# Performance work log

Measured on AMD Instinct MI355X. Metric: run time of the kernel, lower is better.

Reference implementation:

```python
import jax, jax.numpy as jnp
import numpy as np

B, T, I, H = 32, 512, 512, 512  # batch, seq_len, input_size, hidden_size


def setup_inputs() -> dict:
    key = jax.random.key(0)
    ks = jax.random.split(key, 9)
    s = 1.0 / np.sqrt(H)  # PyTorch LSTM init: U(-1/sqrt(H), 1/sqrt(H))
    u = lambda k, shape: jax.random.uniform(k, shape, jnp.float32, -s, s)
    return {
        "x": jax.random.normal(ks[0], (B, T, I), jnp.float32),
        "h0": jnp.zeros((2, B, H), jnp.float32),
        "c0": jnp.zeros((2, B, H), jnp.float32),
        "w_ih_f": u(ks[1], (4 * H, I)), "w_hh_f": u(ks[2], (4 * H, H)),
        "b_ih_f": u(ks[3], (4 * H,)), "b_hh_f": u(ks[4], (4 * H,)),
        "w_ih_r": u(ks[5], (4 * H, I)), "w_hh_r": u(ks[6], (4 * H, H)),
        "b_ih_r": u(ks[7], (4 * H,)), "b_hh_r": u(ks[8], (4 * H,)),
    }


def _lstm_dir(x, h0, c0, w_ih, w_hh, b_ih, b_hh):
    # Precompute input projections for all timesteps: [T, B, 4H] (time-major for scan).
    gx = jnp.einsum('bti,gi->tbg', x, w_ih) + b_ih + b_hh

    def step(carry, g):
        h, c = carry
        g = g + h @ w_hh.T  # [B, 4H]
        i, f, gg, o = jnp.split(g, 4, axis=-1)  # PyTorch gate order: i, f, g, o
        c = jax.nn.sigmoid(f) * c + jax.nn.sigmoid(i) * jnp.tanh(gg)
        h = jax.nn.sigmoid(o) * jnp.tanh(c)
        return (h, c), h

    (hT, cT), hs = jax.lax.scan(step, (h0, c0), gx)
    return hs.transpose(1, 0, 2), hT, cT  # [B, T, H], [B, H], [B, H]


def reference(x, h0, c0, w_ih_f, w_hh_f, b_ih_f, b_hh_f,
              w_ih_r, w_hh_r, b_ih_r, b_hh_r):
    out_f, hT_f, cT_f = _lstm_dir(x, h0[0], c0[0], w_ih_f, w_hh_f, b_ih_f, b_hh_f)
    out_r, hT_r, cT_r = _lstm_dir(x[:, ::-1], h0[1], c0[1], w_ih_r, w_hh_r, b_ih_r, b_hh_r)
    out = jnp.concatenate([out_f, out_r[:, ::-1]], axis=-1)  # [B, T, 2H]
    h_n = jnp.stack([hT_f, hT_r])  # [2, B, H]
    c_n = jnp.stack([cT_f, cT_r])  # [2, B, H]
    return out, h_n, c_n
```

## Files before the change

### kernel.cpp

```cpp
#include <hip/hip_runtime.h>
#include <hip/hip_bf16.h>
#include <math.h>
#include <stdint.h>

#define BB 32
#define TT 512
#define II 512
#define HH 512
#define G4 (4 * HH)
#define MM (TT * BB)
#define BH (BB * HH)
#define WGD 32

typedef __hip_bfloat16 bf16;
typedef __attribute__((ext_vector_type(8))) short short8;
typedef __attribute__((ext_vector_type(4))) float f32x4;
typedef __attribute__((ext_vector_type(4))) unsigned u32x4;

__device__ __forceinline__ float bf2f(bf16 v) { return __bfloat162float(v); }
__device__ __forceinline__ bf16  f2bf(float v) { return __float2bfloat16(v); }
__device__ __forceinline__ short f2bs(float x) { bf16 v = f2bf(x); return *reinterpret_cast<short*>(&v); }
__device__ __forceinline__ float bs2f(short s) {
    unsigned u = ((unsigned)(unsigned short)s) << 16;
    return __uint_as_float(u);
}
__device__ __forceinline__ short8 pk8(float4 u, float4 v) {
    short8 t;
    t[0] = f2bs(u.x); t[1] = f2bs(u.y); t[2] = f2bs(u.z); t[3] = f2bs(u.w);
    t[4] = f2bs(v.x); t[5] = f2bs(v.y); t[6] = f2bs(v.z); t[7] = f2bs(v.w);
    return t;
}

#define GX1 ((size_t)TT * 4 * 128 * 128)

__global__ __launch_bounds__(256) void proj_mfma_kernel(
    const float* __restrict__ x,
    const float* __restrict__ w_f, const float* __restrict__ w_r,
    const float* __restrict__ bi_f, const float* __restrict__ bh_f,
    const float* __restrict__ bi_r, const float* __restrict__ bh_r,
    bf16* __restrict__ gx, int dir0)
{
    const int dl = blockIdx.z, dir = dir0 + dl;
    const int m0 = blockIdx.x * 64;
    const int n0 = blockIdx.y * 128;
    const float* __restrict__ w  = dir ? w_r  : w_f;
    const float* __restrict__ bi = dir ? bi_r : bi_f;
    const float* __restrict__ bh = dir ? bh_r : bh_f;

    __shared__ __align__(16) char smem[17408];
    bf16 (*As)[40]  = (bf16(*)[40])smem;
    bf16 (*Bs)[40]  = (bf16(*)[40])(smem + 5120);
    bf16 (*Cs)[136] = (bf16(*)[136])smem;

    const int tid = threadIdx.x;
    const int wv = tid >> 6, l = tid & 63;
    const int nl = l & 15, ko = (l >> 4) * 8;

    const int a_r = tid >> 2, a_s = tid & 3;
    const float* a_src = x + ((size_t)((m0 + a_r) & 31) * TT + (size_t)((m0 + a_r) >> 5)) * II + a_s * 8;
    const int b_r = tid >> 1, b_h = tid & 1;
    const float* b_src = w + (size_t)(n0 + b_r) * II + b_h * 16;

    f32x4 acc[8];
#pragma unroll
    for (int j = 0; j < 8; ++j) acc[j] = (f32x4){0.f, 0.f, 0.f, 0.f};

    float bias[8];
#pragma unroll
    for (int j = 0; j < 8; ++j) {
        const int n = n0 + j * 16 + nl;
        bias[j] = bi[n] + bh[n];
    }

    for (int k0 = 0; k0 < II; k0 += 32) {
        const float4 av0 = *(const float4*)(a_src + k0);
        const float4 av1 = *(const float4*)(a_src + k0 + 4);
        const float4 bv0 = *(const float4*)(b_src + k0);
        const float4 bv1 = *(const float4*)(b_src + k0 + 4);
        const float4 bv2 = *(const float4*)(b_src + k0 + 8);
        const float4 bv3 = *(const float4*)(b_src + k0 + 12);
        __syncthreads();
        *(short8*)&As[a_r][a_s * 8] = pk8(av0, av1);
        *(short8*)&Bs[b_r][b_h * 16]     = pk8(bv0, bv1);
        *(short8*)&Bs[b_r][b_h * 16 + 8] = pk8(bv2, bv3);
        __syncthreads();
        const short8 a = *(const short8*)&As[wv * 16 + nl][ko];
#pragma unroll
        for (int j = 0; j < 8; ++j) {
            const short8 b = *(const short8*)&Bs[j * 16 + nl][ko];
            acc[j] = __builtin_amdgcn_mfma_f32_16x16x32_bf16(a, b, acc[j], 0, 0, 0);
        }
    }

    __syncthreads();
    const int row0 = (l >> 4) * 4;
#pragma unroll
    for (int j = 0; j < 8; ++j)
#pragma unroll
        for (int r = 0; r < 4; ++r)
            Cs[wv * 16 + row0 + r][j * 16 + nl] = f2bf(acc[j][r] + bias[j]);
    __syncthreads();

    bf16* gxd = gx + (size_t)dl * GX1;
    const int g   = n0 >> 9;
    const int cgb = (n0 & 511) >> 2;
    const int t_base = blockIdx.x * 2;
#pragma unroll
    for (int i = 0; i < 4; ++i) {
        const int c = i * 256 + tid;
        const int tl = c >> 9, cgl = (c >> 4) & 31, u = c & 15;
        const int r0 = tl * 32 + 2 * u;
        const uint2 lo = *(const uint2*)&Cs[r0][cgl * 4];
        const uint2 hi = *(const uint2*)&Cs[r0 + 1][cgl * 4];
        uint4 ov; ov.x = lo.x; ov.y = lo.y; ov.z = hi.x; ov.w = hi.y;
        *(uint4*)(gxd + ((((size_t)(t_base + tl) * 4 + g) * 128 + cgb + cgl) * 128 + u * 8)) = ov;
    }
}

__global__ __launch_bounds__(256, 1) void lstm_rec_kernel(
    const bf16* __restrict__ gx,
    const float* __restrict__ h0, const float* __restrict__ c0,
    const float* __restrict__ whh_f, const float* __restrict__ whh_r,
    float* __restrict__ dout,
    bf16* __restrict__ h_buf,
    unsigned int* __restrict__ bars,
    int dir0)
{
    const int dl  = blockIdx.x >> 5;
    const int wgl = blockIdx.x & 31;
    const int dir = dir0 + dl;
    const int tid = threadIdx.x;
    const int wv  = tid >> 6;
    const int l   = tid & 63;
    const int cg  = wgl * 4 + wv;
    const int j0  = cg * 4;
    const float* __restrict__ whh = dir ? whh_r : whh_f;
    unsigned int* barsd = bars + (size_t)dl * 256;

    __shared__ __align__(16) bf16 h_s[32][520];
    __shared__ __align__(16) float ex[4][16][36];

    const int nl = l & 15;
    const int g  = nl >> 2, jj = nl & 3;
    const int ko = (l >> 4) * 8;

    short8 bfrag[16];
    {
        const float* wr = whh + ((size_t)g * HH + (size_t)(j0 + jj)) * HH;
#pragma unroll
        for (int ks = 0; ks < 16; ++ks) {
            const float* p = wr + ks * 32 + ko;
            short8 t;
#pragma unroll
            for (int i = 0; i < 8; ++i) t[i] = f2bs(p[i]);
            bfrag[ks] = t;
        }
    }

    const int mC = l >> 1;
    const int jjA = (l & 1) * 2;

    float cs0, cs1;
    {
        const float* cp = c0 + (size_t)dir * BH + (size_t)mC * HH + j0 + jjA;
        cs0 = cp[0]; cs1 = cp[1];
    }

    bf16* hsl = h_buf + (size_t)dl * 2 * BH;
    const unsigned* gxw = (const unsigned*)(gx + (size_t)dl * GX1);

    for (int q = 0; q < 64; ++q) {
        const int f = q * 256 + tid;
        h_s[f >> 9][f & 511] = f2bf(h0[(size_t)dir * BH + f]);
    }
    __syncthreads();

    unsigned gw[4];
    {
        const int t0 = dir ? (TT - 1) : 0;
#pragma unroll
        for (int gg = 0; gg < 4; ++gg)
            gw[gg] = gxw[((size_t)(t0 * 4 + gg) * 128 + cg) * 64 + l];
    }

#pragma unroll 1
    for (int s = 0; s < TT; ++s) {
        const int t_x = dir ? (TT - 1 - s) : s;

        f32x4 acc0 = {0.f, 0.f, 0.f, 0.f};
        f32x4 acc1 = {0.f, 0.f, 0.f, 0.f};
#pragma unroll
        for (int half = 0; half < 2; ++half) {
            short8 a0[8], a1[8];
#pragma unroll
            for (int k = 0; k < 8; ++k) {
                const int ks = half * 8 + k;
                a0[k] = *(const short8*)&h_s[nl][ks * 32 + ko];
                a1[k] = *(const short8*)&h_s[nl + 16][ks * 32 + ko];
            }
#pragma unroll
            for (int k = 0; k < 8; ++k) {
                acc0 = __builtin_amdgcn_mfma_f32_16x16x32_bf16(a0[k], bfrag[half * 8 + k], acc0, 0, 0, 0);
                acc1 = __builtin_amdgcn_mfma_f32_16x16x32_bf16(a1[k], bfrag[half * 8 + k], acc1, 0, 0, 0);
            }
        }

        {
            const int row0 = (l >> 4) * 4;
            *(f32x4*)&ex[wv][nl][row0]      = acc0;
            *(f32x4*)&ex[wv][nl][16 + row0] = acc1;
        }

        float hv0, hv1;
#pragma unroll
        for (int c = 0; c < 2; ++c) {
            const int jc = jjA + c;
            const int sh = 16 * c;
            float q0 = ex[wv][0 * 4 + jc][mC] + bs2f((short)(gw[0] >> sh));
            float q1 = ex[wv][1 * 4 + jc][mC] + bs2f((short)(gw[1] >> sh));
            float q2 = ex[wv][2 * 4 + jc][mC] + bs2f((short)(gw[2] >> sh));
            float q3 = ex[wv][3 * 4 + jc][mC] + bs2f((short)(gw[3] >> sh));
            q0 = fminf(fmaxf(q0, -30.f), 30.f);
            q1 = fminf(fmaxf(q1, -30.f), 30.f);
            q2 = fminf(fmaxf(q2, -30.f), 30.f);
            q3 = fminf(fmaxf(q3, -30.f), 30.f);
            const float ig = 1.f / (1.f + __expf(-q0));
            const float fg = 1.f / (1.f + __expf(-q1));
            const float te = __expf(2.f * q2);
            const float gg = (te - 1.f) / (te + 1.f);
            const float og = 1.f / (1.f + __expf(-q3));
            float cs = (c == 0) ? cs0 : cs1;
            cs = fg * cs + ig * gg;
            const float csc = fminf(fmaxf(cs, -15.f), 15.f);
            const float t2 = __expf(2.f * csc);
            const float th = (t2 - 1.f) / (t2 + 1.f);
            const float h = og * th;
            if (c == 0) { cs0 = cs; hv0 = h; } else { cs1 = cs; hv1 = h; }
        }

        if (s < TT - 1) {
            {
                bf16 hb0 = f2bf(hv0), hb1 = f2bf(hv1);
                unsigned pk = (unsigned)*(unsigned short*)&hb0 |
                              ((unsigned)*(unsigned short*)&hb1 << 16);
                unsigned* hp = (unsigned*)(hsl + (size_t)((s + 1) & 1) * BH + (size_t)mC * HH + j0 + jjA);
                __hip_atomic_store(hp, pk, __ATOMIC_RELAXED, __HIP_MEMORY_SCOPE_AGENT);
            }
            asm volatile("s_waitcnt vmcnt(0)" ::: "memory");
            __syncthreads();
            if (tid == 0)
                __hip_atomic_fetch_add(barsd + (wgl & 3) * 64, 1u,
                                       __ATOMIC_RELAXED, __HIP_MEMORY_SCOPE_AGENT);

            {
                float2 ho; ho.x = hv0; ho.y = hv1;
                *(float2*)(dout + ((size_t)mC * TT + t_x) * (2 * HH) + (size_t)dir * HH + j0 + jjA) = ho;
            }
            const int t_n = dir ? (TT - 2 - s) : (s + 1);
            unsigned gwn[4];
#pragma unroll
            for (int gg = 0; gg < 4; ++gg)
                gwn[gg] = gxw[((size_t)(t_n * 4 + gg) * 128 + cg) * 64 + l];

            if (wv == 0 && l < 4) {
                const unsigned tgt = (unsigned)(WGD / 4) * (unsigned)(s + 1);
                while (__hip_atomic_load(barsd + l * 64,
                                         __ATOMIC_RELAXED, __HIP_MEMORY_SCOPE_AGENT) < tgt) {
                    __builtin_amdgcn_s_sleep(1);
                }
            }
            __syncthreads();

            {
                const u32x4* src = (const u32x4*)(hsl + (size_t)((s + 1) & 1) * BH);
                u32x4 vv[8];
#pragma unroll
                for (int q = 0; q < 8; ++q) {
                    const u32x4* p = src + (q * 256 + tid);
                    asm volatile("global_load_dwordx4 %0, %1, off sc0 sc1"
                                 : "=v"(vv[q]) : "v"(p));
                }
                asm volatile("s_waitcnt vmcnt(0)" ::: "memory");
#pragma unroll
                for (int q = 0; q < 8; ++q) {
                    const int e = (q * 256 + tid) * 8;
                    *(u32x4*)&h_s[e >> 9][e & 511] = vv[q];
                }
            }
            __syncthreads();
#pragma unroll
            for (int gg = 0; gg < 4; ++gg) gw[gg] = gwn[gg];
        } else {
            float2 ho; ho.x = hv0; ho.y = hv1;
            *(float2*)(dout + ((size_t)mC * TT + t_x) * (2 * HH) + (size_t)dir * HH + j0 + jjA) = ho;
            const size_t hn_off = (size_t)BB * TT * 2 * HH;
            float2 co; co.x = cs0; co.y = cs1;
            *(float2*)(dout + hn_off + (size_t)dir * BH + (size_t)mC * HH + j0 + jjA) = ho;
            *(float2*)(dout + hn_off + 2 * (size_t)BH + (size_t)dir * BH + (size_t)mC * HH + j0 + jjA) = co;
        }
    }
}

extern "C" void kernel_launch(void* const* d_in, const int* in_sizes, int n_in,
                              void* d_out, int out_size, void* d_ws, size_t ws_size,
                              hipStream_t stream)
{
    (void)in_sizes; (void)n_in; (void)out_size;
    const float* x     = (const float*)d_in[0];
    const float* h0    = (const float*)d_in[1];
    const float* c0    = (const float*)d_in[2];
    const float* wih_f = (const float*)d_in[3];
    const float* whh_f = (const float*)d_in[4];
    const float* bih_f = (const float*)d_in[5];
    const float* bhh_f = (const float*)d_in[6];
    const float* wih_r = (const float*)d_in[7];
    const float* whh_r = (const float*)d_in[8];
    const float* bih_r = (const float*)d_in[9];
    const float* bhh_r = (const float*)d_in[10];
    float* out = (float*)d_out;

    const size_t gx1 = GX1 * sizeof(bf16);
    const size_t needA = 2 * gx1 + (size_t)4 * BH * sizeof(bf16) + 4096;
    char* ws = (char*)d_ws;

    if (ws_size >= needA) {
        bf16* gx = (bf16*)ws;
        bf16* h_buf = (bf16*)(ws + 2 * gx1);
        unsigned int* bars = (unsigned int*)(ws + 2 * gx1 + (size_t)4 * BH * sizeof(bf16));
        hipMemsetAsync(bars, 0, 2048, stream);
        dim3 g1(MM / 64, G4 / 128, 2);
        proj_mfma_kernel<<<g1, 256, 0, stream>>>(x, wih_f, wih_r, bih_f, bhh_f, bih_r, bhh_r, gx, 0);
        lstm_rec_kernel<<<dim3(2 * WGD), dim3(256), 0, stream>>>(
            gx, h0, c0, whh_f, whh_r, out, h_buf, bars, 0);
    } else {
        bf16* gx = (bf16*)ws;
        bf16* h_buf = (bf16*)(ws + gx1);
        unsigned int* bars = (unsigned int*)(ws + gx1 + (size_t)2 * BH * sizeof(bf16));
        for (int d = 0; d < 2; ++d) {
            hipMemsetAsync(bars, 0, 2048, stream);
            dim3 g1(MM / 64, G4 / 128, 1);
            proj_mfma_kernel<<<g1, 256, 0, stream>>>(x, wih_f, wih_r, bih_f, bhh_f, bih_r, bhh_r, gx, d);
            lstm_rec_kernel<<<dim3(WGD), dim3(256), 0, stream>>>(
                gx, h0, c0, whh_f, whh_r, out, h_buf, bars, d);
        }
    }
}
```

Before: 1.867 ms.

## Replace per-step grid barrier with step-tagged ring buffer and flag polling

Each hidden-state pair is stored together with its step number in an 8-slot ring in global memory. Consumers poll those tags directly instead of waiting on a per-step atomic counter barrier, and the full barrier now runs only once every 8 steps to stop slots from being overwritten too early. The goal is to take the grid-wide barrier round trip off the critical path of each recurrence step. In exchange, each exchanged element doubles in size and polling can re-issue loads, which adds memory traffic.

```diff
diff --git a/kernel.cpp b/kernel.cpp
--- a/kernel.cpp
+++ b/kernel.cpp
@@ -11,6 +11,10 @@
 #define MM (TT * BB)
 #define BH (BB * HH)
 #define WGD 32
+
+#define SLOTS 8
+#define PAIRS 8192
+#define RING1 ((size_t)SLOTS * PAIRS * 8)
 
 typedef __hip_bfloat16 bf16;
 typedef __attribute__((ext_vector_type(8))) short short8;
@@ -122,7 +126,7 @@
     const float* __restrict__ h0, const float* __restrict__ c0,
     const float* __restrict__ whh_f, const float* __restrict__ whh_r,
     float* __restrict__ dout,
-    bf16* __restrict__ h_buf,
+    unsigned long long* __restrict__ ring,
     unsigned int* __restrict__ bars,
     int dir0)
 {
@@ -135,6 +139,7 @@
     const int cg  = wgl * 4 + wv;
     const int j0  = cg * 4;
     const float* __restrict__ whh = dir ? whh_r : whh_f;
+    unsigned long long* ringd = ring + (size_t)dl * SLOTS * PAIRS;
     unsigned int* barsd = bars + (size_t)dl * 256;
 
     __shared__ __align__(16) bf16 h_s[32][520];
@@ -157,8 +162,10 @@
         }
     }
 
-    const int mC = l >> 1;
+    const int mC  = l >> 1;
     const int jjA = (l & 1) * 2;
+    const int pc_own = cg * 2 + (l & 1);
+    const bool own_col = (((tid & 127) >> 2) == wgl);
 
     float cs0, cs1;
     {
@@ -166,7 +173,6 @@
         cs0 = cp[0]; cs1 = cp[1];
     }
 
-    bf16* hsl = h_buf + (size_t)dl * 2 * BH;
     const unsigned* gxw = (const unsigned*)(gx + (size_t)dl * GX1);
 
     for (int q = 0; q < 64; ++q) {
@@ -238,19 +244,20 @@
             if (c == 0) { cs0 = cs; hv0 = h; } else { cs1 = cs; hv1 = h; }
         }
 
+        __syncthreads();
+
         if (s < TT - 1) {
+            unsigned pk;
             {
                 bf16 hb0 = f2bf(hv0), hb1 = f2bf(hv1);
-                unsigned pk = (unsigned)*(unsigned short*)&hb0 |
-                              ((unsigned)*(unsigned short*)&hb1 << 16);
-                unsigned* hp = (unsigned*)(hsl + (size_t)((s + 1) & 1) * BH + (size_t)mC * HH + j0 + jjA);
-                __hip_atomic_store(hp, pk, __ATOMIC_RELAXED, __HIP_MEMORY_SCOPE_AGENT);
-            }
-            asm volatile("s_waitcnt vmcnt(0)" ::: "memory");
-            __syncthreads();
-            if (tid == 0)
-                __hip_atomic_fetch_add(barsd + (wgl & 3) * 64, 1u,
-                                       __ATOMIC_RELAXED, __HIP_MEMORY_SCOPE_AGENT);
+                pk = (unsigned)*(unsigned short*)&hb0 |
+                     ((unsigned)*(unsigned short*)&hb1 << 16);
+                const unsigned long long pk64 =
+                    (unsigned long long)pk | ((unsigned long long)(unsigned)(s + 1) << 32);
+                unsigned long long* hp =
+                    ringd + (size_t)((s + 1) & (SLOTS - 1)) * PAIRS + (size_t)mC * 256 + pc_own;
+                __hip_atomic_store(hp, pk64, __ATOMIC_RELAXED, __HIP_MEMORY_SCOPE_AGENT);
+            }
 
             {
                 float2 ho; ho.x = hv0; ho.y = hv1;
@@ -262,32 +269,53 @@
             for (int gg = 0; gg < 4; ++gg)
                 gwn[gg] = gxw[((size_t)(t_n * 4 + gg) * 128 + cg) * 64 + l];
 
-            if (wv == 0 && l < 4) {
-                const unsigned tgt = (unsigned)(WGD / 4) * (unsigned)(s + 1);
-                while (__hip_atomic_load(barsd + l * 64,
-                                         __ATOMIC_RELAXED, __HIP_MEMORY_SCOPE_AGENT) < tgt) {
-                    __builtin_amdgcn_s_sleep(1);
+            {
+                const unsigned expt = (unsigned)(s + 1);
+                const char* sb = (const char*)(ringd + (size_t)((s + 1) & (SLOTS - 1)) * PAIRS)
+                                 + (size_t)tid * 16;
+                const int row_h = tid >> 7;
+                const int bcol  = 4 * (tid & 127);
+                u32x4 vv[16];
+                unsigned need = own_col ? 0u : 0xffffu;
+                while (need) {
+#pragma unroll
+                    for (int q = 0; q < 16; ++q) {
+                        if (need & (1u << q)) {
+                            const char* p = sb + q * 4096;
+                            asm volatile("global_load_dwordx4 %0, %1, off sc0 sc1"
+                                         : "=v"(vv[q]) : "v"(p));
+                        }
+                    }
+                    asm volatile("s_waitcnt vmcnt(0)" ::: "memory");
+#pragma unroll
+                    for (int q = 0; q < 16; ++q) {
+                        if (need & (1u << q)) {
+                            if (vv[q][1] == expt && vv[q][3] == expt) {
+                                uint2 o; o.x = vv[q][0]; o.y = vv[q][2];
+                                *(uint2*)&h_s[2 * q + row_h][bcol] = o;
+                                need &= ~(1u << q);
+                            }
+                        }
+                    }
                 }
+                *(unsigned*)&h_s[mC][j0 + jjA] = pk;
             }
             __syncthreads();
 
-            {
-                const u32x4* src = (const u32x4*)(hsl + (size_t)((s + 1) & 1) * BH);
-                u32x4 vv[8];
-#pragma unroll
-                for (int q = 0; q < 8; ++q) {
-                    const u32x4* p = src + (q * 256 + tid);
-                    asm volatile("global_load_dwordx4 %0, %1, off sc0 sc1"
-                                 : "=v"(vv[q]) : "v"(p));
+            if (((s + 1) & (SLOTS - 1)) == 0) {
+                if (tid == 0)
+                    __hip_atomic_fetch_add(barsd + (wgl & 3) * 64, 1u,
+                                           __ATOMIC_RELAXED, __HIP_MEMORY_SCOPE_AGENT);
+                if (wv == 0 && l < 4) {
+                    const unsigned tgt = (unsigned)(WGD / 4) * (unsigned)((s + 1) >> 3);
+                    while (__hip_atomic_load(barsd + l * 64,
+                                             __ATOMIC_RELAXED, __HIP_MEMORY_SCOPE_AGENT) < tgt) {
+                        __builtin_amdgcn_s_sleep(1);
+                    }
                 }
-                asm volatile("s_waitcnt vmcnt(0)" ::: "memory");
-#pragma unroll
-                for (int q = 0; q < 8; ++q) {
-                    const int e = (q * 256 + tid) * 8;
-                    *(u32x4*)&h_s[e >> 9][e & 511] = vv[q];
-                }
-            }
-            __syncthreads();
+                __syncthreads();
+            }
+
 #pragma unroll
             for (int gg = 0; gg < 4; ++gg) gw[gg] = gwn[gg];
         } else {
@@ -320,28 +348,28 @@
     float* out = (float*)d_out;
 
     const size_t gx1 = GX1 * sizeof(bf16);
-    const size_t needA = 2 * gx1 + (size_t)4 * BH * sizeof(bf16) + 4096;
+    const size_t needA = 2 * gx1 + 2 * RING1 + 8192;
     char* ws = (char*)d_ws;
 
     if (ws_size >= needA) {
         bf16* gx = (bf16*)ws;
-        bf16* h_buf = (bf16*)(ws + 2 * gx1);
-        unsigned int* bars = (unsigned int*)(ws + 2 * gx1 + (size_t)4 * BH * sizeof(bf16));
-        hipMemsetAsync(bars, 0, 2048, stream);
+        unsigned long long* ring = (unsigned long long*)(ws + 2 * gx1);
+        unsigned int* bars = (unsigned int*)(ws + 2 * gx1 + 2 * RING1);
+        hipMemsetAsync(ring, 0, 2 * RING1 + 4096, stream);
         dim3 g1(MM / 64, G4 / 128, 2);
         proj_mfma_kernel<<<g1, 256, 0, stream>>>(x, wih_f, wih_r, bih_f, bhh_f, bih_r, bhh_r, gx, 0);
         lstm_rec_kernel<<<dim3(2 * WGD), dim3(256), 0, stream>>>(
-            gx, h0, c0, whh_f, whh_r, out, h_buf, bars, 0);
+            gx, h0, c0, whh_f, whh_r, out, ring, bars, 0);
     } else {
         bf16* gx = (bf16*)ws;
-        bf16* h_buf = (bf16*)(ws + gx1);
-        unsigned int* bars = (unsigned int*)(ws + gx1 + (size_t)2 * BH * sizeof(bf16));
+        unsigned long long* ring = (unsigned long long*)(ws + gx1);
+        unsigned int* bars = (unsigned int*)(ws + gx1 + RING1);
         for (int d = 0; d < 2; ++d) {
-            hipMemsetAsync(bars, 0, 2048, stream);
+            hipMemsetAsync(ring, 0, RING1 + 4096, stream);
             dim3 g1(MM / 64, G4 / 128, 1);
             proj_mfma_kernel<<<g1, 256, 0, stream>>>(x, wih_f, wih_r, bih_f, bhh_f, bih_r, bhh_r, gx, d);
             lstm_rec_kernel<<<dim3(WGD), dim3(256), 0, stream>>>(
-                gx, h0, c0, whh_f, whh_r, out, h_buf, bars, d);
-        }
-    }
-}
+                gx, h0, c0, whh_f, whh_r, out, ring, bars, d);
+        }
+    }
+}
```

Result: slower. 2.264 ms (+21.3%).

## Replace per-step grid barrier with NaN-sentinel ring buffer polling for hidden state

Applied to the files above, without the earlier changes.

Swaps the per-timestep atomic-counter grid barrier for a ring buffer with one slot per timestep. Each slot is pre-filled with bf16 NaN sentinels, and consumers poll the slot until every 16-byte chunk is non-NaN, so the counter round-trip and the spin-wait are gone from the critical path. Each workgroup writes its own chunk straight into LDS instead of reading it back. In exchange the kernel must initialise a much larger ring buffer up front, uses more workspace, and would misbehave if a real hidden value were the NaN pattern.

```diff
diff --git a/kernel.cpp b/kernel.cpp
--- a/kernel.cpp
+++ b/kernel.cpp
@@ -11,6 +11,11 @@
 #define MM (TT * BB)
 #define BH (BB * HH)
 #define WGD 32
+
+#define SLOT_DW (BH / 2)
+#define RING_DW ((size_t)TT * SLOT_DW)
+#define RING_BYTES (RING_DW * 4)
+#define NANP 0x7FC0u
 
 typedef __hip_bfloat16 bf16;
 typedef __attribute__((ext_vector_type(8))) short short8;
@@ -122,7 +127,7 @@
     const float* __restrict__ h0, const float* __restrict__ c0,
     const float* __restrict__ whh_f, const float* __restrict__ whh_r,
     float* __restrict__ dout,
-    bf16* __restrict__ h_buf,
+    unsigned* __restrict__ ring,
     unsigned int* __restrict__ bars,
     int dir0)
 {
@@ -135,6 +140,7 @@
     const int cg  = wgl * 4 + wv;
     const int j0  = cg * 4;
     const float* __restrict__ whh = dir ? whh_r : whh_f;
+    unsigned* ringd = ring + (size_t)dl * RING_DW;
     unsigned int* barsd = bars + (size_t)dl * 256;
 
     __shared__ __align__(16) bf16 h_s[32][520];
@@ -157,8 +163,9 @@
         }
     }
 
-    const int mC = l >> 1;
+    const int mC  = l >> 1;
     const int jjA = (l & 1) * 2;
+    const int poff = mC * 256 + ((j0 + jjA) >> 1);
 
     float cs0, cs1;
     {
@@ -166,13 +173,33 @@
         cs0 = cp[0]; cs1 = cp[1];
     }
 
-    bf16* hsl = h_buf + (size_t)dl * 2 * BH;
     const unsigned* gxw = (const unsigned*)(gx + (size_t)dl * GX1);
 
     for (int q = 0; q < 64; ++q) {
         const int f = q * 256 + tid;
         h_s[f >> 9][f & 511] = f2bf(h0[(size_t)dir * BH + f]);
     }
+
+    {
+        unsigned long long* rq = (unsigned long long*)ringd;
+        const int gt = wgl * 256 + tid;
+        const unsigned long long NN = 0x7FC07FC07FC07FC0ull;
+#pragma unroll 4
+        for (int q = 0; q < 256; ++q)
+            __hip_atomic_store(rq + (size_t)q * 8192 + gt, NN,
+                               __ATOMIC_RELAXED, __HIP_MEMORY_SCOPE_AGENT);
+        asm volatile("s_waitcnt vmcnt(0)" ::: "memory");
+    }
+    __syncthreads();
+    if (tid == 0)
+        __hip_atomic_fetch_add(barsd + (wgl & 3) * 64, 1u,
+                               __ATOMIC_RELAXED, __HIP_MEMORY_SCOPE_AGENT);
+    if (wv == 0 && l < 4) {
+        while (__hip_atomic_load(barsd + l * 64,
+                                 __ATOMIC_RELAXED, __HIP_MEMORY_SCOPE_AGENT) < (unsigned)(WGD / 4)) {
+            __builtin_amdgcn_s_sleep(1);
+        }
+    }
     __syncthreads();
 
     unsigned gw[4];
@@ -182,6 +209,8 @@
         for (int gg = 0; gg < 4; ++gg)
             gw[gg] = gxw[((size_t)(t0 * 4 + gg) * 128 + cg) * 64 + l];
     }
+
+    const unsigned need_init = (((tid & 63) >> 1) == wgl) ? 0u : 0xFFu;
 
 #pragma unroll 1
     for (int s = 0; s < TT; ++s) {
@@ -238,19 +267,19 @@
             if (c == 0) { cs0 = cs; hv0 = h; } else { cs1 = cs; hv1 = h; }
         }
 
+        __syncthreads();
+
         if (s < TT - 1) {
+            unsigned* slot = ringd + (size_t)(s + 1) * SLOT_DW;
+
+            unsigned pk;
             {
                 bf16 hb0 = f2bf(hv0), hb1 = f2bf(hv1);
-                unsigned pk = (unsigned)*(unsigned short*)&hb0 |
-                              ((unsigned)*(unsigned short*)&hb1 << 16);
-                unsigned* hp = (unsigned*)(hsl + (size_t)((s + 1) & 1) * BH + (size_t)mC * HH + j0 + jjA);
-                __hip_atomic_store(hp, pk, __ATOMIC_RELAXED, __HIP_MEMORY_SCOPE_AGENT);
-            }
-            asm volatile("s_waitcnt vmcnt(0)" ::: "memory");
-            __syncthreads();
-            if (tid == 0)
-                __hip_atomic_fetch_add(barsd + (wgl & 3) * 64, 1u,
-                                       __ATOMIC_RELAXED, __HIP_MEMORY_SCOPE_AGENT);
+                pk = (unsigned)*(unsigned short*)&hb0 |
+                     ((unsigned)*(unsigned short*)&hb1 << 16);
+                __hip_atomic_store(slot + poff, pk,
+                                   __ATOMIC_RELAXED, __HIP_MEMORY_SCOPE_AGENT);
+            }
 
             {
                 float2 ho; ho.x = hv0; ho.y = hv1;
@@ -262,30 +291,36 @@
             for (int gg = 0; gg < 4; ++gg)
                 gwn[gg] = gxw[((size_t)(t_n * 4 + gg) * 128 + cg) * 64 + l];
 
-            if (wv == 0 && l < 4) {
-                const unsigned tgt = (unsigned)(WGD / 4) * (unsigned)(s + 1);
-                while (__hip_atomic_load(barsd + l * 64,
-                                         __ATOMIC_RELAXED, __HIP_MEMORY_SCOPE_AGENT) < tgt) {
-                    __builtin_amdgcn_s_sleep(1);
+            {
+                u32x4 vv[8];
+                unsigned need = need_init;
+                while (need) {
+#pragma unroll
+                    for (int q = 0; q < 8; ++q) {
+                        if (need & (1u << q)) {
+                            const unsigned* p = slot + (q * 256 + tid) * 4;
+                            asm volatile("global_load_dwordx4 %0, %1, off sc0 sc1"
+                                         : "=v"(vv[q]) : "v"(p));
+                        }
+                    }
+                    asm volatile("s_waitcnt vmcnt(0)" ::: "memory");
+#pragma unroll
+                    for (int q = 0; q < 8; ++q) {
+                        if (need & (1u << q)) {
+                            const u32x4 v = vv[q];
+                            const bool ok = ((v[0] & 0xffffu) != NANP) &
+                                            ((v[1] & 0xffffu) != NANP) &
+                                            ((v[2] & 0xffffu) != NANP) &
+                                            ((v[3] & 0xffffu) != NANP);
+                            if (ok) {
+                                const int c = q * 256 + tid;
+                                *(u32x4*)&h_s[c >> 6][(c & 63) * 8] = v;
+                                need &= ~(1u << q);
+                            }
+                        }
+                    }
                 }
-            }
-            __syncthreads();
-
-            {
-                const u32x4* src = (const u32x4*)(hsl + (size_t)((s + 1) & 1) * BH);
-                u32x4 vv[8];
-#pragma unroll
-                for (int q = 0; q < 8; ++q) {
-                    const u32x4* p = src + (q * 256 + tid);
-                    asm volatile("global_load_dwordx4 %0, %1, off sc0 sc1"
-                                 : "=v"(vv[q]) : "v"(p));
-                }
-                asm volatile("s_waitcnt vmcnt(0)" ::: "memory");
-#pragma unroll
-                for (int q = 0; q < 8; ++q) {
-                    const int e = (q * 256 + tid) * 8;
-                    *(u32x4*)&h_s[e >> 9][e & 511] = vv[q];
-                }
+                *(unsigned*)&h_s[mC][j0 + jjA] = pk;
             }
             __syncthreads();
 #pragma unroll
@@ -320,28 +355,28 @@
     float* out = (float*)d_out;
 
     const size_t gx1 = GX1 * sizeof(bf16);
-    const size_t needA = 2 * gx1 + (size_t)4 * BH * sizeof(bf16) + 4096;
+    const size_t needA = 2 * gx1 + 2 * RING_BYTES + 8192;
     char* ws = (char*)d_ws;
 
     if (ws_size >= needA) {
         bf16* gx = (bf16*)ws;
-        bf16* h_buf = (bf16*)(ws + 2 * gx1);
-        unsigned int* bars = (unsigned int*)(ws + 2 * gx1 + (size_t)4 * BH * sizeof(bf16));
-        hipMemsetAsync(bars, 0, 2048, stream);
+        unsigned* ring = (unsigned*)(ws + 2 * gx1);
+        unsigned int* bars = (unsigned int*)(ws + 2 * gx1 + 2 * RING_BYTES);
+        hipMemsetAsync(bars, 0, 4096, stream);
         dim3 g1(MM / 64, G4 / 128, 2);
         proj_mfma_kernel<<<g1, 256, 0, stream>>>(x, wih_f, wih_r, bih_f, bhh_f, bih_r, bhh_r, gx, 0);
         lstm_rec_kernel<<<dim3(2 * WGD), dim3(256), 0, stream>>>(
-            gx, h0, c0, whh_f, whh_r, out, h_buf, bars, 0);
+            gx, h0, c0, whh_f, whh_r, out, ring, bars, 0);
     } else {
         bf16* gx = (bf16*)ws;
-        bf16* h_buf = (bf16*)(ws + gx1);
-        unsigned int* bars = (unsigned int*)(ws + gx1 + (size_t)2 * BH * sizeof(bf16));
+        unsigned* ring = (unsigned*)(ws + gx1);
+        unsigned int* bars = (unsigned int*)(ws + gx1 + RING_BYTES);
         for (int d = 0; d < 2; ++d) {
-            hipMemsetAsync(bars, 0, 2048, stream);
+            hipMemsetAsync(bars, 0, 4096, stream);
             dim3 g1(MM / 64, G4 / 128, 1);
             proj_mfma_kernel<<<g1, 256, 0, stream>>>(x, wih_f, wih_r, bih_f, bhh_f, bih_r, bhh_r, gx, d);
             lstm_rec_kernel<<<dim3(WGD), dim3(256), 0, stream>>>(
-                gx, h0, c0, whh_f, whh_r, out, h_buf, bars, d);
-        }
-    }
-}
+                gx, h0, c0, whh_f, whh_r, out, ring, bars, d);
+        }
+    }
+}
```

Result: slower. 2.211 ms (+18.4%).

## Run both LSTM directions in one workgroup set sharing a per-step grid barrier

Applied to the files above, without the earlier changes.

Adds a recurrent kernel where each of 32 workgroups handles both the forward and reverse direction for its hidden slice. Both directions share one cross-workgroup barrier per timestep instead of using 64 workgroups with one barrier set per direction. This halves the number of participating workgroups and interleaves the two cells' work, aiming to cut barrier and launch overhead per step. In exchange each workgroup holds twice the register weights and LDS and does twice the serial work per step, so per-step latency grows and register pressure may cause spills.

```diff
diff --git a/kernel.cpp b/kernel.cpp
--- a/kernel.cpp
+++ b/kernel.cpp
@@ -114,6 +114,231 @@
         const uint2 hi = *(const uint2*)&Cs[r0 + 1][cgl * 4];
         uint4 ov; ov.x = lo.x; ov.y = lo.y; ov.z = hi.x; ov.w = hi.y;
         *(uint4*)(gxd + ((((size_t)(t_base + tl) * 4 + g) * 128 + cgb + cgl) * 128 + u * 8)) = ov;
+    }
+}
+
+__device__ __forceinline__ void cell_step(
+    const bf16 (*__restrict__ h_s)[520], const short8* __restrict__ bfrag,
+    float (*__restrict__ exw)[36],
+    const unsigned* __restrict__ gw,
+    int nl, int ko, int l, int mC, int jjA,
+    float& cs0, float& cs1, float& hv0, float& hv1)
+{
+    f32x4 acc0 = {0.f, 0.f, 0.f, 0.f};
+    f32x4 acc1 = {0.f, 0.f, 0.f, 0.f};
+#pragma unroll
+    for (int half = 0; half < 2; ++half) {
+        short8 a0[8], a1[8];
+#pragma unroll
+        for (int k = 0; k < 8; ++k) {
+            const int ks = half * 8 + k;
+            a0[k] = *(const short8*)&h_s[nl][ks * 32 + ko];
+            a1[k] = *(const short8*)&h_s[nl + 16][ks * 32 + ko];
+        }
+#pragma unroll
+        for (int k = 0; k < 8; ++k) {
+            acc0 = __builtin_amdgcn_mfma_f32_16x16x32_bf16(a0[k], bfrag[half * 8 + k], acc0, 0, 0, 0);
+            acc1 = __builtin_amdgcn_mfma_f32_16x16x32_bf16(a1[k], bfrag[half * 8 + k], acc1, 0, 0, 0);
+        }
+    }
+    const int row0 = (l >> 4) * 4;
+    *(f32x4*)&exw[nl][row0]      = acc0;
+    *(f32x4*)&exw[nl][16 + row0] = acc1;
+
+#pragma unroll
+    for (int c = 0; c < 2; ++c) {
+        const int jc = jjA + c;
+        const int sh = 16 * c;
+        float q0 = exw[0 * 4 + jc][mC] + bs2f((short)(gw[0] >> sh));
+        float q1 = exw[1 * 4 + jc][mC] + bs2f((short)(gw[1] >> sh));
+        float q2 = exw[2 * 4 + jc][mC] + bs2f((short)(gw[2] >> sh));
+        float q3 = exw[3 * 4 + jc][mC] + bs2f((short)(gw[3] >> sh));
+        q0 = fminf(fmaxf(q0, -30.f), 30.f);
+        q1 = fminf(fmaxf(q1, -30.f), 30.f);
+        q2 = fminf(fmaxf(q2, -30.f), 30.f);
+        q3 = fminf(fmaxf(q3, -30.f), 30.f);
+        const float ig = 1.f / (1.f + __expf(-q0));
+        const float fg = 1.f / (1.f + __expf(-q1));
+        const float te = __expf(2.f * q2);
+        const float gg = (te - 1.f) / (te + 1.f);
+        const float og = 1.f / (1.f + __expf(-q3));
+        float cs = (c == 0) ? cs0 : cs1;
+        cs = fg * cs + ig * gg;
+        const float csc = fminf(fmaxf(cs, -15.f), 15.f);
+        const float t2 = __expf(2.f * csc);
+        const float th = (t2 - 1.f) / (t2 + 1.f);
+        const float h = og * th;
+        if (c == 0) { cs0 = cs; hv0 = h; } else { cs1 = cs; hv1 = h; }
+    }
+}
+
+__global__ __launch_bounds__(256, 1) void lstm_rec2_kernel(
+    const bf16* __restrict__ gx,
+    const float* __restrict__ h0, const float* __restrict__ c0,
+    const float* __restrict__ whh_f, const float* __restrict__ whh_r,
+    float* __restrict__ dout,
+    bf16* __restrict__ h_buf,
+    unsigned int* __restrict__ bars)
+{
+    const int wgl = blockIdx.x;
+    const int tid = threadIdx.x;
+    const int wv  = tid >> 6;
+    const int l   = tid & 63;
+    const int cg  = wgl * 4 + wv;
+    const int j0  = cg * 4;
+
+    __shared__ __align__(16) bf16 h_sf[32][520];
+    __shared__ __align__(16) bf16 h_sr[32][520];
+    __shared__ __align__(16) float ex[4][16][36];
+
+    const int nl = l & 15;
+    const int g  = nl >> 2, jj = nl & 3;
+    const int ko = (l >> 4) * 8;
+
+    short8 bfF[16], bfR[16];
+    {
+        const size_t roff = ((size_t)g * HH + (size_t)(j0 + jj)) * HH;
+        const float* wrF = whh_f + roff;
+        const float* wrR = whh_r + roff;
+#pragma unroll
+        for (int ks = 0; ks < 16; ++ks) {
+            const float* pF = wrF + ks * 32 + ko;
+            const float* pR = wrR + ks * 32 + ko;
+            short8 tF, tR;
+#pragma unroll
+            for (int i = 0; i < 8; ++i) { tF[i] = f2bs(pF[i]); tR[i] = f2bs(pR[i]); }
+            bfF[ks] = tF; bfR[ks] = tR;
+        }
+    }
+
+    const int mC  = l >> 1;
+    const int jjA = (l & 1) * 2;
+
+    float csF0, csF1, csR0, csR1;
+    {
+        const float* cpF = c0 + (size_t)mC * HH + j0 + jjA;
+        const float* cpR = c0 + (size_t)BH + (size_t)mC * HH + j0 + jjA;
+        csF0 = cpF[0]; csF1 = cpF[1];
+        csR0 = cpR[0]; csR1 = cpR[1];
+    }
+
+    bf16* hbF = h_buf;
+    bf16* hbR = h_buf + 2 * BH;
+    const unsigned* gxF = (const unsigned*)gx;
+    const unsigned* gxR = (const unsigned*)(gx + GX1);
+
+    for (int q = 0; q < 64; ++q) {
+        const int f = q * 256 + tid;
+        h_sf[f >> 9][f & 511] = f2bf(h0[f]);
+        h_sr[f >> 9][f & 511] = f2bf(h0[BH + f]);
+    }
+    __syncthreads();
+
+    unsigned gwF[4], gwR[4];
+#pragma unroll
+    for (int gg = 0; gg < 4; ++gg) {
+        gwF[gg] = gxF[((size_t)(0 * 4 + gg) * 128 + cg) * 64 + l];
+        gwR[gg] = gxR[((size_t)((TT - 1) * 4 + gg) * 128 + cg) * 64 + l];
+    }
+
+#pragma unroll 1
+    for (int s = 0; s < TT; ++s) {
+        float hvF0, hvF1;
+        cell_step(h_sf, bfF, ex[wv], gwF, nl, ko, l, mC, jjA, csF0, csF1, hvF0, hvF1);
+
+        unsigned pkF = 0, pkR = 0;
+        if (s < TT - 1) {
+            bf16 hb0 = f2bf(hvF0), hb1 = f2bf(hvF1);
+            pkF = (unsigned)*(unsigned short*)&hb0 |
+                  ((unsigned)*(unsigned short*)&hb1 << 16);
+            unsigned* hp = (unsigned*)(hbF + (size_t)((s + 1) & 1) * BH + (size_t)mC * HH + j0 + jjA);
+            __hip_atomic_store(hp, pkF, __ATOMIC_RELAXED, __HIP_MEMORY_SCOPE_AGENT);
+        }
+
+        float hvR0, hvR1;
+        cell_step(h_sr, bfR, ex[wv], gwR, nl, ko, l, mC, jjA, csR0, csR1, hvR0, hvR1);
+
+        if (s < TT - 1) {
+            {
+                bf16 hb0 = f2bf(hvR0), hb1 = f2bf(hvR1);
+                pkR = (unsigned)*(unsigned short*)&hb0 |
+                      ((unsigned)*(unsigned short*)&hb1 << 16);
+                unsigned* hp = (unsigned*)(hbR + (size_t)((s + 1) & 1) * BH + (size_t)mC * HH + j0 + jjA);
+                __hip_atomic_store(hp, pkR, __ATOMIC_RELAXED, __HIP_MEMORY_SCOPE_AGENT);
+            }
+            asm volatile("s_waitcnt vmcnt(0)" ::: "memory");
+            __syncthreads();
+            if (tid == 0)
+                __hip_atomic_fetch_add(bars + (wgl & 3) * 64, 1u,
+                                       __ATOMIC_RELAXED, __HIP_MEMORY_SCOPE_AGENT);
+
+            {
+                float2 ho; ho.x = hvF0; ho.y = hvF1;
+                *(float2*)(dout + ((size_t)mC * TT + s) * (2 * HH) + j0 + jjA) = ho;
+                float2 hr; hr.x = hvR0; hr.y = hvR1;
+                *(float2*)(dout + ((size_t)mC * TT + (TT - 1 - s)) * (2 * HH) + HH + j0 + jjA) = hr;
+            }
+            unsigned gwnF[4], gwnR[4];
+#pragma unroll
+            for (int gg = 0; gg < 4; ++gg) {
+                gwnF[gg] = gxF[((size_t)((s + 1) * 4 + gg) * 128 + cg) * 64 + l];
+                gwnR[gg] = gxR[((size_t)((TT - 2 - s) * 4 + gg) * 128 + cg) * 64 + l];
+            }
+
+            if (wv == 0 && l < 4) {
+                const unsigned tgt = (unsigned)(WGD / 4) * (unsigned)(s + 1);
+                while (__hip_atomic_load(bars + l * 64,
+                                         __ATOMIC_RELAXED, __HIP_MEMORY_SCOPE_AGENT) < tgt) {
+                    __builtin_amdgcn_s_sleep(1);
+                }
+            }
+            __syncthreads();
+
+            {
+                const u32x4* srcF = (const u32x4*)(hbF + (size_t)((s + 1) & 1) * BH);
+                const u32x4* srcR = (const u32x4*)(hbR + (size_t)((s + 1) & 1) * BH);
+                u32x4 vf[8], vr[8];
+#pragma unroll
+                for (int q = 0; q < 8; ++q) {
+                    const u32x4* p = srcF + (q * 256 + tid);
+                    asm volatile("global_load_dwordx4 %0, %1, off sc0 sc1"
+                                 : "=v"(vf[q]) : "v"(p));
+                }
+#pragma unroll
+                for (int q = 0; q < 8; ++q) {
+                    const u32x4* p = srcR + (q * 256 + tid);
+                    asm volatile("global_load_dwordx4 %0, %1, off sc0 sc1"
+                                 : "=v"(vr[q]) : "v"(p));
+                }
+                asm volatile("s_waitcnt vmcnt(0)" ::: "memory");
+#pragma unroll
+                for (int q = 0; q < 8; ++q) {
+                    const int e = (q * 256 + tid) * 8;
+                    *(u32x4*)&h_sf[e >> 9][e & 511] = vf[q];
+                }
+#pragma unroll
+                for (int q = 0; q < 8; ++q) {
+                    const int e = (q * 256 + tid) * 8;
+                    *(u32x4*)&h_sr[e >> 9][e & 511] = vr[q];
+                }
+            }
+            __syncthreads();
+#pragma unroll
+            for (int gg = 0; gg < 4; ++gg) { gwF[gg] = gwnF[gg]; gwR[gg] = gwnR[gg]; }
+        } else {
+            const size_t hn_off = (size_t)BB * TT * 2 * HH;
+            float2 ho; ho.x = hvF0; ho.y = hvF1;
+            *(float2*)(dout + ((size_t)mC * TT + (TT - 1)) * (2 * HH) + j0 + jjA) = ho;
+            *(float2*)(dout + hn_off + (size_t)mC * HH + j0 + jjA) = ho;
+            float2 cf; cf.x = csF0; cf.y = csF1;
+            *(float2*)(dout + hn_off + 2 * (size_t)BH + (size_t)mC * HH + j0 + jjA) = cf;
+
+            float2 hr; hr.x = hvR0; hr.y = hvR1;
+            *(float2*)(dout + ((size_t)mC * TT + 0) * (2 * HH) + HH + j0 + jjA) = hr;
+            *(float2*)(dout + hn_off + (size_t)BH + (size_t)mC * HH + j0 + jjA) = hr;
+            float2 cr; cr.x = csR0; cr.y = csR1;
+            *(float2*)(dout + hn_off + 3 * (size_t)BH + (size_t)mC * HH + j0 + jjA) = cr;
+        }
     }
 }
 
@@ -187,56 +412,8 @@
     for (int s = 0; s < TT; ++s) {
         const int t_x = dir ? (TT - 1 - s) : s;
 
-        f32x4 acc0 = {0.f, 0.f, 0.f, 0.f};
-        f32x4 acc1 = {0.f, 0.f, 0.f, 0.f};
-#pragma unroll
-        for (int half = 0; half < 2; ++half) {
-            short8 a0[8], a1[8];
-#pragma unroll
-            for (int k = 0; k < 8; ++k) {
-                const int ks = half * 8 + k;
-                a0[k] = *(const short8*)&h_s[nl][ks * 32 + ko];
-                a1[k] = *(const short8*)&h_s[nl + 16][ks * 32 + ko];
-            }
-#pragma unroll
-            for (int k = 0; k < 8; ++k) {
-                acc0 = __builtin_amdgcn_mfma_f32_16x16x32_bf16(a0[k], bfrag[half * 8 + k], acc0, 0, 0, 0);
-                acc1 = __builtin_amdgcn_mfma_f32_16x16x32_bf16(a1[k], bfrag[half * 8 + k], acc1, 0, 0, 0);
-            }
-        }
-
-        {
-            const int row0 = (l >> 4) * 4;
-            *(f32x4*)&ex[wv][nl][row0]      = acc0;
-            *(f32x4*)&ex[wv][nl][16 + row0] = acc1;
-        }
-
         float hv0, hv1;
-#pragma unroll
-        for (int c = 0; c < 2; ++c) {
-            const int jc = jjA + c;
-            const int sh = 16 * c;
-            float q0 = ex[wv][0 * 4 + jc][mC] + bs2f((short)(gw[0] >> sh));
-            float q1 = ex[wv][1 * 4 + jc][mC] + bs2f((short)(gw[1] >> sh));
-            float q2 = ex[wv][2 * 4 + jc][mC] + bs2f((short)(gw[2] >> sh));
-            float q3 = ex[wv][3 * 4 + jc][mC] + bs2f((short)(gw[3] >> sh));
-            q0 = fminf(fmaxf(q0, -30.f), 30.f);
-            q1 = fminf(fmaxf(q1, -30.f), 30.f);
-            q2 = fminf(fmaxf(q2, -30.f), 30.f);
-            q3 = fminf(fmaxf(q3, -30.f), 30.f);
-            const float ig = 1.f / (1.f + __expf(-q0));
-            const float fg = 1.f / (1.f + __expf(-q1));
-            const float te = __expf(2.f * q2);
-            const float gg = (te - 1.f) / (te + 1.f);
-            const float og = 1.f / (1.f + __expf(-q3));
-            float cs = (c == 0) ? cs0 : cs1;
-            cs = fg * cs + ig * gg;
-            const float csc = fminf(fmaxf(cs, -15.f), 15.f);
-            const float t2 = __expf(2.f * csc);
-            const float th = (t2 - 1.f) / (t2 + 1.f);
-            const float h = og * th;
-            if (c == 0) { cs0 = cs; hv0 = h; } else { cs1 = cs; hv1 = h; }
-        }
+        cell_step(h_s, bfrag, ex[wv], gw, nl, ko, l, mC, jjA, cs0, cs1, hv0, hv1);
 
         if (s < TT - 1) {
             {
@@ -330,8 +507,8 @@
         hipMemsetAsync(bars, 0, 2048, stream);
         dim3 g1(MM / 64, G4 / 128, 2);
         proj_mfma_kernel<<<g1, 256, 0, stream>>>(x, wih_f, wih_r, bih_f, bhh_f, bih_r, bhh_r, gx, 0);
-        lstm_rec_kernel<<<dim3(2 * WGD), dim3(256), 0, stream>>>(
-            gx, h0, c0, whh_f, whh_r, out, h_buf, bars, 0);
+        lstm_rec2_kernel<<<dim3(WGD), dim3(256), 0, stream>>>(
+            gx, h0, c0, whh_f, whh_r, out, h_buf, bars);
     } else {
         bf16* gx = (bf16*)ws;
         bf16* h_buf = (bf16*)(ws + gx1);
```

Measured after the change: 2.931 ms. 57.0% more time.
